# Kernel tuning notes

Measured on AMD Instinct MI355X. Metric: run time of the kernel, lower is better.

Reference implementation:

```python
import jax, jax.numpy as jnp
import numpy as np

N_NODES = 100000
N_EDGES = 1600000
IN_FEATS = 64
N_CLASSES = 64


def setup_inputs() -> dict:
    key = jax.random.key(0)
    k1, k2, k3, k4, k5 = jax.random.split(key, 5)
    feat = jax.random.normal(k1, (N_NODES, IN_FEATS), dtype=jnp.float32)
    edge_row = jnp.sort(jax.random.randint(k2, (N_EDGES,), 0, N_NODES))
    edge_col = jax.random.randint(k3, (N_EDGES,), 0, N_NODES)
    # values of the cached normalized adjacency power (all positive, ~1/deg scale)
    edge_val = jax.random.uniform(k4, (N_EDGES,), dtype=jnp.float32) / 16.0
    # nn.Linear(in_feats, n_classes): weight [C, F] (xavier), bias zeros
    limit = float(np.sqrt(6.0 / (IN_FEATS + N_CLASSES)))
    W = jax.random.uniform(k5, (N_CLASSES, IN_FEATS), dtype=jnp.float32,
                           minval=-limit, maxval=limit)
    b = jnp.zeros((N_CLASSES,), dtype=jnp.float32)
    return {"feat": feat, "edge_row": edge_row, "edge_col": edge_col,
            "edge_val": edge_val, "W": W, "b": b}


def reference(feat, edge_row, edge_col, edge_val, W, b):
    # SpMM: h = A_pre @ feat, A_pre given as COO (edge_row, edge_col, edge_val)
    msg = edge_val[:, None] * feat[edge_col]          # [E, F] gather + scale
    h = jax.ops.segment_sum(msg, edge_row, num_segments=N_NODES)  # [N, F]
    # fc: Linear(in_feats -> n_classes), norm=None so no normalization
    return h @ W.T + b                                 # [N, C]
```

## Files before the change

### kernel.cpp

```cpp
#include <hip/hip_runtime.h>
#include <hip/hip_bf16.h>

typedef __attribute__((ext_vector_type(8))) short short8;
typedef __attribute__((ext_vector_type(4))) float f32x4;

__device__ __forceinline__ unsigned short f2bf(float x) {
    unsigned int u = __float_as_uint(x);
    unsigned int lsb = (u >> 16) & 1u;
    u += 0x7fffu + lsb;
    return (unsigned short)(u >> 16);
}

__device__ __forceinline__ short8 pack8(f32x4 a, f32x4 b) {
    short8 r;
    r[0] = (short)f2bf(a.x); r[1] = (short)f2bf(a.y);
    r[2] = (short)f2bf(a.z); r[3] = (short)f2bf(a.w);
    r[4] = (short)f2bf(b.x); r[5] = (short)f2bf(b.y);
    r[6] = (short)f2bf(b.z); r[7] = (short)f2bf(b.w);
    return r;
}

__global__ __launch_bounds__(256) void k_init(const float* __restrict__ bias,
                                              float* __restrict__ out, long total4) {
    long i4 = (long)blockIdx.x * 256 + threadIdx.x;
    if (i4 < total4) {
        const f32x4* b4 = (const f32x4*)bias;
        ((f32x4*)out)[i4] = b4[i4 & 15];
    }
}

__global__ __launch_bounds__(256) void k_setup(const float* __restrict__ feat,
                                               const float* __restrict__ W,
                                               const float* __restrict__ bias,
                                               unsigned short* __restrict__ G,
                                               float* __restrict__ out,
                                               int N, int gblocks) {
    if ((int)blockIdx.x >= gblocks) {
        long i4 = (long)(blockIdx.x - gblocks) * 256 + threadIdx.x;
        long total4 = (long)N * 16;
        if (i4 < total4) {
            const f32x4* b4 = (const f32x4*)bias;
            ((f32x4*)out)[i4] = b4[i4 & 15];
        }
        return;
    }

    int wave = blockIdx.x * 4 + (threadIdx.x >> 6);
    int lane = threadIdx.x & 63;
    int m0 = wave * 16;
    if (m0 >= N) return;
    int n = lane & 15;
    int quad = lane >> 4;

    short8 bf[4][2];
#pragma unroll
    for (int ct = 0; ct < 4; ++ct)
#pragma unroll
        for (int ks = 0; ks < 2; ++ks) {
            const f32x4* wp = (const f32x4*)(W + (size_t)(ct * 16 + n) * 64 + ks * 32 + quad * 8);
            f32x4 w0 = wp[0];
            f32x4 w1 = wp[1];
            bf[ct][ks] = pack8(w0, w1);
        }

    int mrow = m0 + n; if (mrow >= N) mrow = N - 1;
    short8 af[2];
#pragma unroll
    for (int ks = 0; ks < 2; ++ks) {
        const f32x4* ap = (const f32x4*)(feat + (size_t)mrow * 64 + ks * 32 + quad * 8);
        f32x4 a0 = __builtin_nontemporal_load(ap);
        f32x4 a1 = __builtin_nontemporal_load(ap + 1);
        af[ks] = pack8(a0, a1);
    }

    f32x4 acc[4];
#pragma unroll
    for (int ct = 0; ct < 4; ++ct) {
        acc[ct] = (f32x4){0.f, 0.f, 0.f, 0.f};
#pragma unroll
        for (int ks = 0; ks < 2; ++ks)
            acc[ct] = __builtin_amdgcn_mfma_f32_16x16x32_bf16(af[ks], bf[ct][ks], acc[ct], 0, 0, 0);
    }

    size_t pstride = (size_t)N * 16;
#pragma unroll
    for (int ct = 0; ct < 4; ++ct)
#pragma unroll
        for (int r = 0; r < 4; ++r) {
            int rowm = m0 + quad * 4 + r;
            if (rowm < N)
                G[(size_t)ct * pstride + (size_t)rowm * 16 + n] = f2bf(acc[ct][r]);
        }
}

__global__ __launch_bounds__(256) void k_spmm(const unsigned short* __restrict__ G,
                                              const int* __restrict__ erow,
                                              const int* __restrict__ ecol,
                                              const float* __restrict__ evalv,
                                              const float* __restrict__ bias,
                                              float* __restrict__ out, int E, int N) {
    int b = blockIdx.x;
    int fg  = (b & 7) >> 1;
    int sub = (b >> 3) * 2 + (b & 1);
    int wavein = threadIdx.x >> 6;
    int lane = threadIdx.x & 63;
    long base0 = ((long)sub * 4 + wavein) * 256;
    if (base0 >= E) return;

    int fb = lane & 15;
    int q  = lane >> 4;
    int vq4 = q << 2;
    const unsigned short* plane = G + (size_t)fg * ((size_t)N * 16);
    float blane = bias[fg * 16 + fb];

    float acc = 0.f;
    bool first = true;
    int cur;

    auto flush = [&](bool atomic_path) {
        float t = acc + __shfl_xor(acc, 16);
        t += __shfl_xor(t, 32);
        if (lane < 16) {
            float* p = out + ((size_t)(unsigned)cur << 6) + (unsigned)(fg * 16 + lane);
            if (atomic_path) atomicAdd(p, t);
            else *p = blane + t;
        }
        acc = 0.f;
    };

    if (base0 + 256 <= E) {
        long i0 = base0 + lane;
        int rv[4], cv[4], vv[4];
#pragma unroll
        for (int c = 0; c < 4; ++c) {
            rv[c] = __builtin_nontemporal_load(erow + i0 + 64 * c);
            cv[c] = __builtin_nontemporal_load(ecol + i0 + 64 * c);
            vv[c] = __builtin_nontemporal_load((const int*)evalv + i0 + 64 * c);
        }
        cur = __builtin_amdgcn_readlane(rv[0], 0);

        unsigned long long bm[4];
#pragma unroll
        for (int c = 0; c < 4; ++c) {
            int rn = __shfl_down(rv[c], 1);
            unsigned long long m = __ballot(rv[c] != rn) & 0x7fffffffffffffffULL;
            int r63 = __builtin_amdgcn_readlane(rv[c], 63);
            int n0  = (c < 3) ? __builtin_amdgcn_readlane(rv[c + 1], 0) : (r63 + 1);
            if (r63 != n0) m |= 0x8000000000000000ULL;
            bm[c] = m;
        }

        unsigned gbuf[2][8];
#pragma unroll
        for (int k = 0; k < 8; ++k) {
            int c0 = __builtin_amdgcn_ds_bpermute(vq4 + 16 * k, cv[0]);
            gbuf[0][k] = plane[(size_t)(unsigned)c0 * 16 + fb];
        }

        bool prevb = false;
#pragma unroll
        for (int g = 0; g < 8; ++g) {
            if (g < 7) {
                const int cn = (g + 1) >> 1;
#pragma unroll
                for (int k = 0; k < 8; ++k) {
                    const int pj = ((g + 1) & 1) * 8 + k;
                    int cc = __builtin_amdgcn_ds_bpermute(vq4 + 16 * pj, cv[cn]);
                    gbuf[(g + 1) & 1][k] = plane[(size_t)(unsigned)cc * 16 + fb];
                }
            }
            __builtin_amdgcn_sched_barrier(0);

#pragma unroll
            for (int k = 0; k < 8; ++k) {
                const int p  = g * 8 + k;
                const int c  = p >> 4;
                const int j  = p & 15;
                const int i4 = j * 4;
                float vs = __int_as_float(__builtin_amdgcn_ds_bpermute(vq4 + i4 * 4, vv[c]));
                float f  = __uint_as_float(gbuf[g & 1][k] << 16);
                bool slow = (j == 0) ? (prevb || (bm[c] & 7ULL) != 0)
                                     : (((bm[c] >> (4 * j - 1)) & 0xFULL) != 0);
                if (!slow) {
                    acc = fmaf(vs, f, acc);
                } else {
                    int r0 = __builtin_amdgcn_readlane(rv[c], i4);
                    int r3 = __builtin_amdgcn_readlane(rv[c], i4 + 3);
                    if (r0 == r3) {
                        if (r0 != cur) { flush(first); first = false; cur = r0; }
                        acc = fmaf(vs, f, acc);
                    } else {
                        int rowsv = __builtin_amdgcn_ds_bpermute(vq4 + i4 * 4, rv[c]);
                        int r1 = __builtin_amdgcn_readlane(rv[c], i4 + 1);
                        int r2 = __builtin_amdgcn_readlane(rv[c], i4 + 2);
                        int rr = r0;
                        while (true) {
                            if (rr != cur) { flush(first); first = false; cur = rr; }
                            float vm = (rowsv == rr) ? vs : 0.f;
                            acc = fmaf(vm, f, acc);
                            if (rr == r3) break;
                            rr = (r1 > rr) ? r1 : ((r2 > rr) ? r2 : r3);
                        }
                    }
                }
                if (j == 15 && p < 63) prevb = ((bm[c] >> 63) & 1ULL) != 0;
            }
        }
    } else {
        cur = erow[base0];
        for (long e = base0; e < (long)E; ++e) {
            int r = erow[e];
            int c = ecol[e];
            float v = evalv[e];
            float f = __uint_as_float((unsigned)plane[(size_t)(unsigned)c * 16 + fb] << 16);
            if (r != cur) { flush(first); first = false; cur = r; }
            float vm = (q == 0) ? v : 0.f;
            acc = fmaf(vm, f, acc);
        }
    }

    flush(true);
}

__global__ __launch_bounds__(256) void k_fused(const float* __restrict__ feat,
                                               const int* __restrict__ erow,
                                               const int* __restrict__ ecol,
                                               const float* __restrict__ evalv,
                                               const float* __restrict__ W,
                                               float* __restrict__ out,
                                               int E, int epw) {
    __shared__ float Wt[64 * 64];
    for (int i = threadIdx.x; i < 4096; i += 256) {
        int c = i >> 6, f = i & 63;
        Wt[f * 64 + c] = W[i];
    }
    __syncthreads();

    int wave = blockIdx.x * 4 + (threadIdx.x >> 6);
    int lane = threadIdx.x & 63;
    long e0 = (long)wave * epw;
    if (e0 >= E) return;
    long e1 = e0 + epw; if (e1 > E) e1 = E;

    int cur = erow[e0];
    float acc = 0.f;
    for (long e = e0; e < e1; ++e) {
        int r = erow[e];
        int c = ecol[e];
        float v = evalv[e];
        float g = feat[((size_t)c << 6) | lane];
        if (r != cur) {
            float res = 0.f;
#pragma unroll
            for (int f = 0; f < 64; ++f)
                res += __shfl(acc, f, 64) * Wt[f * 64 + lane];
            atomicAdd(out + ((size_t)cur << 6) + lane, res);
            acc = 0.f;
            cur = r;
        }
        acc += v * g;
    }
    {
        float res = 0.f;
#pragma unroll
        for (int f = 0; f < 64; ++f)
            res += __shfl(acc, f, 64) * Wt[f * 64 + lane];
        atomicAdd(out + ((size_t)cur << 6) + lane, res);
    }
}

extern "C" void kernel_launch(void* const* d_in, const int* in_sizes, int n_in,
                              void* d_out, int out_size, void* d_ws, size_t ws_size,
                              hipStream_t stream) {
    const float* feat  = (const float*)d_in[0];
    const int*   erow  = (const int*)d_in[1];
    const int*   ecol  = (const int*)d_in[2];
    const float* evalv = (const float*)d_in[3];
    const float* W     = (const float*)d_in[4];
    const float* bias  = (const float*)d_in[5];
    float* out = (float*)d_out;

    int N = in_sizes[0] / 64;
    int E = in_sizes[1];

    size_t need = (size_t)N * 64 * sizeof(unsigned short);
    if (ws_size >= need) {
        unsigned short* G = (unsigned short*)d_ws;
        int tiles = (N + 15) / 16;
        int gblocks = (tiles + 3) / 4;
        long total4 = (long)N * 16;
        int iblocks = (int)((total4 + 255) / 256);
        k_setup<<<gblocks + iblocks, 256, 0, stream>>>(feat, W, bias, G, out, N, gblocks);

        int nwpf = (E + 255) / 256;
        int bpf  = (nwpf + 3) / 4;
        int noct = (bpf + 1) / 2;
        k_spmm<<<noct * 8, 256, 0, stream>>>(G, erow, ecol, evalv, bias, out, E, N);
    } else {
        long total4 = (long)N * 16;
        k_init<<<(int)((total4 + 255) / 256), 256, 0, stream>>>(bias, out, total4);
        int epw = (E + 8191) / 8192;
        if (epw < 32) epw = 32;
        int nwaves = (E + epw - 1) / epw;
        int nblocks = (nwaves + 3) / 4;
        k_fused<<<nblocks, 256, 0, stream>>>(feat, erow, ecol, evalv, W, out, E, epw);
    }
}
```

Baseline: 173.7 us.

## Switch G to row-major layout and gather two features per lane in SpMM

The projected-feature buffer G moves from four 16-column planes to a row-major [N,64] bf16 layout. Each SpMM lane now loads a 32-bit pair of bf16 features and keeps two accumulators, so each block covers 32 output columns and the column-group count drops from four to two. The gather prefetch is deepened from double to triple buffering. The aim is fewer passes over the edge list (fewer edge-index reloads and bpermutes), at the cost of more registers and wider per-row gathers.

```diff
diff --git a/kernel.cpp b/kernel.cpp
--- a/kernel.cpp
+++ b/kernel.cpp
@@ -82,14 +82,13 @@
             acc[ct] = __builtin_amdgcn_mfma_f32_16x16x32_bf16(af[ks], bf[ct][ks], acc[ct], 0, 0, 0);
     }
 
-    size_t pstride = (size_t)N * 16;
 #pragma unroll
     for (int ct = 0; ct < 4; ++ct)
 #pragma unroll
         for (int r = 0; r < 4; ++r) {
             int rowm = m0 + quad * 4 + r;
             if (rowm < N)
-                G[(size_t)ct * pstride + (size_t)rowm * 16 + n] = f2bf(acc[ct][r]);
+                G[(size_t)rowm * 64 + ct * 16 + n] = f2bf(acc[ct][r]);
         }
 }
 
@@ -98,44 +97,60 @@
                                               const int* __restrict__ ecol,
                                               const float* __restrict__ evalv,
                                               const float* __restrict__ bias,
-                                              float* __restrict__ out, int E, int N) {
+                                              float* __restrict__ out, int E) {
     int b = blockIdx.x;
-    int fg  = (b & 7) >> 1;
-    int sub = (b >> 3) * 2 + (b & 1);
+    int fg  = (b & 7) >> 2;
+    int sub = (b >> 3) * 4 + (b & 3);
     int wavein = threadIdx.x >> 6;
     int lane = threadIdx.x & 63;
     long base0 = ((long)sub * 4 + wavein) * 256;
     if (base0 >= E) return;
 
-    int fb = lane & 15;
     int q  = lane >> 4;
+    int fs = lane & 15;
     int vq4 = q << 2;
-    const unsigned short* plane = G + (size_t)fg * ((size_t)N * 16);
-    float blane = bias[fg * 16 + fb];
-
-    float acc = 0.f;
+    unsigned voff = (unsigned)fs * 4u;
+    const char* Gb = (const char*)G + ((unsigned)fg << 6);
+    float2 b2 = ((const float2*)bias)[fg * 16 + fs];
+
+    float acc0 = 0.f, acc1 = 0.f;
     bool first = true;
     int cur;
 
-    auto flush = [&](bool atomic_path) {
-        float t = acc + __shfl_xor(acc, 16);
-        t += __shfl_xor(t, 32);
+    auto flush_atomic = [&]() {
+        float t0 = acc0 + __shfl_xor(acc0, 16);
+        float t1 = acc1 + __shfl_xor(acc1, 16);
+        t0 += __shfl_xor(t0, 32);
+        t1 += __shfl_xor(t1, 32);
         if (lane < 16) {
-            float* p = out + ((size_t)(unsigned)cur << 6) + (unsigned)(fg * 16 + lane);
-            if (atomic_path) atomicAdd(p, t);
-            else *p = blane + t;
-        }
-        acc = 0.f;
+            float* p = out + ((size_t)(unsigned)cur << 6) + (unsigned)(fg * 32 + fs * 2);
+            atomicAdd(p, t0);
+            atomicAdd(p + 1, t1);
+        }
+        acc0 = 0.f; acc1 = 0.f;
+    };
+    auto flush = [&]() {
+        if (first) { flush_atomic(); first = false; return; }
+        float t0 = acc0 + __shfl_xor(acc0, 16);
+        float t1 = acc1 + __shfl_xor(acc1, 16);
+        t0 += __shfl_xor(t0, 32);
+        t1 += __shfl_xor(t1, 32);
+        if (lane < 16) {
+            float* p = out + ((size_t)(unsigned)cur << 6) + (unsigned)(fg * 32 + fs * 2);
+            float2 o; o.x = b2.x + t0; o.y = b2.y + t1;
+            *(float2*)p = o;
+        }
+        acc0 = 0.f; acc1 = 0.f;
     };
 
     if (base0 + 256 <= E) {
         long i0 = base0 + lane;
-        int rv[4], cv[4], vv[4];
+        int rv[4], cv[4], vvv[4];
 #pragma unroll
         for (int c = 0; c < 4; ++c) {
-            rv[c] = __builtin_nontemporal_load(erow + i0 + 64 * c);
-            cv[c] = __builtin_nontemporal_load(ecol + i0 + 64 * c);
-            vv[c] = __builtin_nontemporal_load((const int*)evalv + i0 + 64 * c);
+            rv[c]  = __builtin_nontemporal_load(erow + i0 + 64 * c);
+            cv[c]  = __builtin_nontemporal_load(ecol + i0 + 64 * c);
+            vvv[c] = __builtin_nontemporal_load((const int*)evalv + i0 + 64 * c);
         }
         cur = __builtin_amdgcn_readlane(rv[0], 0);
 
@@ -150,76 +165,86 @@
             bm[c] = m;
         }
 
-        unsigned gbuf[2][8];
-#pragma unroll
-        for (int k = 0; k < 8; ++k) {
-            int c0 = __builtin_amdgcn_ds_bpermute(vq4 + 16 * k, cv[0]);
-            gbuf[0][k] = plane[(size_t)(unsigned)c0 * 16 + fb];
-        }
-
-        bool prevb = false;
+        unsigned gbuf[3][8];
+
+#define SPMM_ISSUE(GI, SLOT) do {                                              \
+    _Pragma("unroll")                                                          \
+    for (int k_ = 0; k_ < 8; ++k_) {                                           \
+        const int p_  = (GI) * 8 + k_;                   \
+        const int c_  = p_ >> 4;                                    \
+        const int pj_ = p_ & 15;                        \
+        int idx_ = vq4 + 16 * pj_;                                             \
+        int colv_ = __builtin_amdgcn_ds_bpermute(idx_, cv[c_]);                \
+        unsigned off_ = ((unsigned)colv_ << 7) + voff;                         \
+        gbuf[SLOT][k_] = *(const unsigned*)(Gb + off_);                        \
+    } } while (0)
+
+        SPMM_ISSUE(0, 0);
+        SPMM_ISSUE(1, 1);
+
 #pragma unroll
         for (int g = 0; g < 8; ++g) {
-            if (g < 7) {
-                const int cn = (g + 1) >> 1;
-#pragma unroll
-                for (int k = 0; k < 8; ++k) {
-                    const int pj = ((g + 1) & 1) * 8 + k;
-                    int cc = __builtin_amdgcn_ds_bpermute(vq4 + 16 * pj, cv[cn]);
-                    gbuf[(g + 1) & 1][k] = plane[(size_t)(unsigned)cc * 16 + fb];
-                }
-            }
+            if (g < 6) SPMM_ISSUE(g + 2, (g + 2) % 3);
             __builtin_amdgcn_sched_barrier(0);
 
 #pragma unroll
             for (int k = 0; k < 8; ++k) {
                 const int p  = g * 8 + k;
                 const int c  = p >> 4;
-                const int j  = p & 15;
-                const int i4 = j * 4;
-                float vs = __int_as_float(__builtin_amdgcn_ds_bpermute(vq4 + i4 * 4, vv[c]));
-                float f  = __uint_as_float(gbuf[g & 1][k] << 16);
-                bool slow = (j == 0) ? (prevb || (bm[c] & 7ULL) != 0)
-                                     : (((bm[c] >> (4 * j - 1)) & 0xFULL) != 0);
+                const int pj = p & 15;
+                const int i4 = pj * 4;
+                int idx = vq4 + i4 * 4;
+                float vs = __int_as_float(__builtin_amdgcn_ds_bpermute(idx, vvv[c]));
+                unsigned u = gbuf[g % 3][k];
+                float flo = __uint_as_float(u << 16);
+                float fhi = __uint_as_float(u & 0xffff0000u);
+                bool slow = (pj == 0) ? ((c > 0 && ((bm[c - 1] >> 63) & 1ULL)) || (bm[c] & 7ULL) != 0)
+                                      : (((bm[c] >> (4 * pj - 1)) & 0xFULL) != 0);
                 if (!slow) {
-                    acc = fmaf(vs, f, acc);
+                    acc0 = fmaf(vs, flo, acc0);
+                    acc1 = fmaf(vs, fhi, acc1);
                 } else {
                     int r0 = __builtin_amdgcn_readlane(rv[c], i4);
                     int r3 = __builtin_amdgcn_readlane(rv[c], i4 + 3);
                     if (r0 == r3) {
-                        if (r0 != cur) { flush(first); first = false; cur = r0; }
-                        acc = fmaf(vs, f, acc);
+                        if (r0 != cur) { flush(); cur = r0; }
+                        acc0 = fmaf(vs, flo, acc0);
+                        acc1 = fmaf(vs, fhi, acc1);
                     } else {
-                        int rowsv = __builtin_amdgcn_ds_bpermute(vq4 + i4 * 4, rv[c]);
+                        int rowsv = __builtin_amdgcn_ds_bpermute(idx, rv[c]);
                         int r1 = __builtin_amdgcn_readlane(rv[c], i4 + 1);
                         int r2 = __builtin_amdgcn_readlane(rv[c], i4 + 2);
                         int rr = r0;
                         while (true) {
-                            if (rr != cur) { flush(first); first = false; cur = rr; }
+                            if (rr != cur) { flush(); cur = rr; }
                             float vm = (rowsv == rr) ? vs : 0.f;
-                            acc = fmaf(vm, f, acc);
+                            acc0 = fmaf(vm, flo, acc0);
+                            acc1 = fmaf(vm, fhi, acc1);
                             if (rr == r3) break;
                             rr = (r1 > rr) ? r1 : ((r2 > rr) ? r2 : r3);
                         }
                     }
                 }
-                if (j == 15 && p < 63) prevb = ((bm[c] >> 63) & 1ULL) != 0;
             }
         }
+#undef SPMM_ISSUE
     } else {
         cur = erow[base0];
         for (long e = base0; e < (long)E; ++e) {
             int r = erow[e];
             int c = ecol[e];
             float v = evalv[e];
-            float f = __uint_as_float((unsigned)plane[(size_t)(unsigned)c * 16 + fb] << 16);
-            if (r != cur) { flush(first); first = false; cur = r; }
+            unsigned u = *(const unsigned*)(Gb + (((unsigned)c << 7) + voff));
+            float flo = __uint_as_float(u << 16);
+            float fhi = __uint_as_float(u & 0xffff0000u);
+            if (r != cur) { flush(); cur = r; }
             float vm = (q == 0) ? v : 0.f;
-            acc = fmaf(vm, f, acc);
-        }
-    }
-
-    flush(true);
+            acc0 = fmaf(vm, flo, acc0);
+            acc1 = fmaf(vm, fhi, acc1);
+        }
+    }
+
+    flush_atomic();
 }
 
 __global__ __launch_bounds__(256) void k_fused(const float* __restrict__ feat,
@@ -294,8 +319,8 @@
 
         int nwpf = (E + 255) / 256;
         int bpf  = (nwpf + 3) / 4;
-        int noct = (bpf + 1) / 2;
-        k_spmm<<<noct * 8, 256, 0, stream>>>(G, erow, ecol, evalv, bias, out, E, N);
+        int noct = (bpf + 3) / 4;
+        k_spmm<<<noct * 8, 256, 0, stream>>>(G, erow, ecol, evalv, bias, out, E);
     } else {
         long total4 = (long)N * 16;
         k_init<<<(int)((total4 + 255) / 256), 256, 0, stream>>>(bias, out, total4);
```

Measured after the change: 164.8 us. 5.1% less time.
